# Kernel optimization log

Measured on AMD Instinct MI355X. Metric: run time of the kernel, lower is better.

## Reference

```python
import jax, jax.numpy as jnp
import numpy as np

D_IN = 768
D_OUT = 768
NUM_HEADS = 12
HEAD_DIM = D_OUT // NUM_HEADS
SEQ = 4096
BATCH = 1


def setup_inputs() -> dict:
    key = jax.random.key(0)
    ks = jax.random.split(key, 6)
    s = 1.0 / np.sqrt(D_IN)
    return {
        "x": jax.random.normal(ks[0], (BATCH, SEQ, D_IN), dtype=jnp.float32),
        "W_query": jax.random.normal(ks[1], (D_IN, D_OUT), dtype=jnp.float32) * s,
        "W_key": jax.random.normal(ks[2], (D_IN, D_OUT), dtype=jnp.float32) * s,
        "W_value": jax.random.normal(ks[3], (D_IN, D_OUT), dtype=jnp.float32) * s,
        "W_out": jax.random.normal(ks[4], (D_OUT, D_OUT), dtype=jnp.float32) * s,
        "b_out": jax.random.normal(ks[5], (D_OUT,), dtype=jnp.float32) * 0.01,
    }


def reference(x, W_query, W_key, W_value, W_out, b_out):
    B, S, _ = x.shape
    # QKV projections (qkv_bias=False)
    q = (x @ W_query).reshape(B, S, NUM_HEADS, HEAD_DIM)
    k = (x @ W_key).reshape(B, S, NUM_HEADS, HEAD_DIM)
    v = (x @ W_value).reshape(B, S, NUM_HEADS, HEAD_DIM)
    # attention scores [B, H, S, S] with causal mask
    scores = jnp.einsum("bqhd,bkhd->bhqk", q, k) / jnp.sqrt(
        jnp.asarray(HEAD_DIM, dtype=x.dtype)
    )
    causal = jnp.tril(jnp.ones((S, S), dtype=bool))
    scores = jnp.where(causal, scores, jnp.finfo(x.dtype).min)
    attn = jax.nn.softmax(scores, axis=-1)  # dropout p=0.0 -> identity
    ctx = jnp.einsum("bhqk,bkhd->bqhd", attn, v).reshape(B, S, D_OUT)
    return ctx @ W_out + b_out
```

## Files before the change

kernel.cpp:

```cpp
#include <hip/hip_runtime.h>
#include <stdint.h>

#define SEQ 4096
#define DM 768
#define NH 12
#define HD 64

typedef __attribute__((ext_vector_type(8))) short bf8;
typedef __attribute__((ext_vector_type(4))) float f4;
typedef __attribute__((ext_vector_type(16))) float f32x16;

static __device__ __forceinline__ f4 mfma_bf16(bf8 a, bf8 b, f4 c) {
  return __builtin_amdgcn_mfma_f32_16x16x32_bf16(a, b, c, 0, 0, 0);
}
static __device__ __forceinline__ f32x16 mfma32(bf8 a, bf8 b, f32x16 c) {
  return __builtin_amdgcn_mfma_f32_32x32x16_bf16(a, b, c, 0, 0, 0);
}

static __device__ __forceinline__ unsigned short f2bf(float f) {
  unsigned int u = __float_as_uint(f);
  u += 0x7FFFu + ((u >> 16) & 1u);
  return (unsigned short)(u >> 16);
}

static __device__ __forceinline__ unsigned int cvtpk(float lo, float hi) {
  unsigned int r;
  asm("v_cvt_pk_bf16_f32 %0, %1, %2" : "=v"(r) : "v"(lo), "v"(hi));
  return r;
}

static __device__ __forceinline__ void gload_lds16(const void* g, void* l) {
  __builtin_amdgcn_global_load_lds(
      (const __attribute__((address_space(1))) void*)g,
      (__attribute__((address_space(3))) void*)l, 16, 0, 0);
}

__global__ __launch_bounds__(256) void k_cvt(const float* __restrict__ x,
                                             unsigned short* __restrict__ xb) {
  int i = (blockIdx.x * 256 + threadIdx.x) * 4;
  float4 v = *reinterpret_cast<const float4*>(x + i);
  ushort4 o;
  o.x = f2bf(v.x); o.y = f2bf(v.y); o.z = f2bf(v.z); o.w = f2bf(v.w);
  *reinterpret_cast<ushort4*>(xb + i) = o;
}

__global__ __launch_bounds__(256) void k_tw(const float* __restrict__ w0,
                                            const float* __restrict__ w1,
                                            const float* __restrict__ w2,
                                            const float* __restrict__ w3,
                                            unsigned short* __restrict__ wt) {
  const float* W = blockIdx.z == 0 ? w0 : blockIdx.z == 1 ? w1
                 : blockIdx.z == 2 ? w2 : w3;
  unsigned short* WT = wt + (size_t)blockIdx.z * DM * DM;
  __shared__ float t[32][33];
  int c0 = blockIdx.x * 32, r0 = blockIdx.y * 32;
  int lx = threadIdx.x & 31, ly = threadIdx.x >> 5;
#pragma unroll
  for (int rr = 0; rr < 32; rr += 8)
    t[ly + rr][lx] = W[(size_t)(r0 + ly + rr) * DM + c0 + lx];
  __syncthreads();
#pragma unroll
  for (int rr = 0; rr < 32; rr += 8)
    WT[(size_t)(c0 + ly + rr) * DM + r0 + lx] = f2bf(t[lx][ly + rr]);
}

template <int MODE>
__global__ __launch_bounds__(256) void k_gemm(const unsigned short* __restrict__ A,
                                              const unsigned short* __restrict__ Bt,
                                              void* __restrict__ Cout,
                                              const float* __restrict__ bias,
                                              float scale) {
  constexpr int K = DM;
  __shared__ unsigned short sA[128 * 32];
  __shared__ unsigned short sB[64 * 32];
  const int t = threadIdx.x, lane = t & 63, w = t >> 6;
  const int wr = w >> 1, wc = w & 1;
  const int c = lane & 15, g = lane >> 4;
  const int brow = blockIdx.x * 128, bcol = blockIdx.y * 64;
  f4 acc[4][2] = {};
  for (int k0 = 0; k0 < K; k0 += 32) {
#pragma unroll
    for (int i = 0; i < 2; ++i) {
      int slot = w * 2 + i;
      int chunk = slot * 64 + lane;
      int row = chunk >> 2;
      int sl = (chunk & 3) ^ ((row >> 1) & 3);
      gload_lds16(A + (size_t)(brow + row) * K + k0 + sl * 8, &sA[slot * 512]);
    }
    {
      int chunk = w * 64 + lane;
      int row = chunk >> 2;
      int sl = (chunk & 3) ^ ((row >> 1) & 3);
      gload_lds16(Bt + (size_t)(bcol + row) * K + k0 + sl * 8, &sB[w * 512]);
    }
    __syncthreads();
    bf8 af[4], bfr[2];
#pragma unroll
    for (int m = 0; m < 4; ++m) {
      int row = wr * 64 + m * 16 + c;
      int off = row * 64 + ((g * 16) ^ (((row >> 1) & 3) << 4));
      af[m] = *reinterpret_cast<const bf8*>(reinterpret_cast<const char*>(sA) + off);
    }
#pragma unroll
    for (int n = 0; n < 2; ++n) {
      int row = wc * 32 + n * 16 + c;
      int off = row * 64 + ((g * 16) ^ (((row >> 1) & 3) << 4));
      bfr[n] = *reinterpret_cast<const bf8*>(reinterpret_cast<const char*>(sB) + off);
    }
#pragma unroll
    for (int m = 0; m < 4; ++m)
#pragma unroll
      for (int n = 0; n < 2; ++n)
        acc[m][n] = mfma_bf16(af[m], bfr[n], acc[m][n]);
    __syncthreads();
  }
#pragma unroll
  for (int m = 0; m < 4; ++m) {
#pragma unroll
    for (int n = 0; n < 2; ++n) {
      int col = bcol + wc * 32 + n * 16 + c;
      int row0 = brow + wr * 64 + m * 16 + g * 4;
      if (MODE == 0) {
        unsigned short* C = (unsigned short*)Cout;
        int h = col >> 6, d = col & 63;
#pragma unroll
        for (int r = 0; r < 4; ++r)
          C[((size_t)h * SEQ + row0 + r) * 64 + d] = f2bf(acc[m][n][r] * scale);
      } else if (MODE == 1) {
        unsigned short* C = (unsigned short*)Cout;
        ushort4 p;
        p.x = f2bf(acc[m][n][0]); p.y = f2bf(acc[m][n][1]);
        p.z = f2bf(acc[m][n][2]); p.w = f2bf(acc[m][n][3]);
        *reinterpret_cast<ushort4*>(C + (size_t)col * SEQ + row0) = p;
      } else {
        float* C = (float*)Cout;
#pragma unroll
        for (int r = 0; r < 4; ++r)
          C[(size_t)(row0 + r) * DM + col] = acc[m][n][r] + bias[col];
      }
    }
  }
}

#define PSWAP(a, b) asm volatile("v_permlane32_swap_b32 %0, %1" : "+v"(a), "+v"(b))

#define STAGEK(tile) do {                                                     \
    const unsigned short* ks_ = Khp + (size_t)(tile) * 4096 + kLaneOff;       \
    _Pragma("unroll")                                                         \
    for (int j_ = 0; j_ < 8; ++j_)                                            \
      gload_lds16(ks_ + j_ * 512, kbuf + j_ * 1024);                          \
  } while (0)

#define ALOADV8(a0, a1) do {                                                  \
    asm volatile("global_load_dwordx4 %0, %1, off"           : "=v"(vf[0]) : "v"(a0)); \
    asm volatile("global_load_dwordx4 %0, %1, off offset:32" : "=v"(vf[1]) : "v"(a0)); \
    asm volatile("global_load_dwordx4 %0, %1, off offset:64" : "=v"(vf[2]) : "v"(a0)); \
    asm volatile("global_load_dwordx4 %0, %1, off offset:96" : "=v"(vf[3]) : "v"(a0)); \
    asm volatile("global_load_dwordx4 %0, %1, off"           : "=v"(vf[4]) : "v"(a1)); \
    asm volatile("global_load_dwordx4 %0, %1, off offset:32" : "=v"(vf[5]) : "v"(a1)); \
    asm volatile("global_load_dwordx4 %0, %1, off offset:64" : "=v"(vf[6]) : "v"(a1)); \
    asm volatile("global_load_dwordx4 %0, %1, off offset:96" : "=v"(vf[7]) : "v"(a1)); \
  } while (0)

#define PBUILD(sv, pfx, pfy) do {                                             \
    float p0_ = __builtin_amdgcn_exp2f(sv[0] - mn_);                          \
    float p1_ = __builtin_amdgcn_exp2f(sv[1] - mn_);                          \
    float p2_ = __builtin_amdgcn_exp2f(sv[2] - mn_);                          \
    float p3_ = __builtin_amdgcn_exp2f(sv[3] - mn_);                          \
    float p4_ = __builtin_amdgcn_exp2f(sv[4] - mn_);                          \
    float p5_ = __builtin_amdgcn_exp2f(sv[5] - mn_);                          \
    float p6_ = __builtin_amdgcn_exp2f(sv[6] - mn_);                          \
    float p7_ = __builtin_amdgcn_exp2f(sv[7] - mn_);                          \
    unsigned int wa0_ = cvtpk(p0_, p1_), wa1_ = cvtpk(p2_, p3_);              \
    unsigned int wb0_ = cvtpk(p4_, p5_), wb1_ = cvtpk(p6_, p7_);              \
    ls_ += ((p0_ + p1_) + (p2_ + p3_)) + ((p4_ + p5_) + (p6_ + p7_));         \
    float q0_ = __builtin_amdgcn_exp2f(sv[8] - mn_);                          \
    float q1_ = __builtin_amdgcn_exp2f(sv[9] - mn_);                          \
    float q2_ = __builtin_amdgcn_exp2f(sv[10] - mn_);                         \
    float q3_ = __builtin_amdgcn_exp2f(sv[11] - mn_);                         \
    float q4_ = __builtin_amdgcn_exp2f(sv[12] - mn_);                         \
    float q5_ = __builtin_amdgcn_exp2f(sv[13] - mn_);                         \
    float q6_ = __builtin_amdgcn_exp2f(sv[14] - mn_);                         \
    float q7_ = __builtin_amdgcn_exp2f(sv[15] - mn_);                         \
    unsigned int wc0_ = cvtpk(q0_, q1_), wc1_ = cvtpk(q2_, q3_);              \
    unsigned int wd0_ = cvtpk(q4_, q5_), wd1_ = cvtpk(q6_, q7_);              \
    ls_ += ((q0_ + q1_) + (q2_ + q3_)) + ((q4_ + q5_) + (q6_ + q7_));         \
    PSWAP(wa0_, wb0_);                                                        \
    PSWAP(wa1_, wb1_);                                                        \
    PSWAP(wc0_, wd0_);                                                        \
    PSWAP(wc1_, wd1_);                                                        \
    uint4 u0_ = {wa0_, wa1_, wb0_, wb1_};                                     \
    uint4 u1_ = {wc0_, wc1_, wd0_, wd1_};                                     \
    pfx = *reinterpret_cast<bf8*>(&u0_);                                      \
    pfy = *reinterpret_cast<bf8*>(&u1_);                                      \
  } while (0)

#define STEP64(t) do {                                                        \
    bf8 vf[8];                                                                \
    const uint64_t va0_ = Vb0a + (uint64_t)(t) * 128;                         \
    const uint64_t va1_ = Vb1a + (uint64_t)(t) * 128;                         \
    ALOADV8(va0_, va1_);                                                      \
    asm volatile("s_waitcnt vmcnt(8)" ::: "memory");                          \
    f32x16 s0_ = {}, s1_ = {};                                                \
    {                                                                         \
      const char* kr0_ = kbuf + ql * 128;                                     \
      const char* kr1_ = kbuf + (32 + ql) * 128;                              \
      const int x0_ = ((hi) ^ xq) << 4;                                       \
      const int x1_ = ((2 + hi) ^ xq) << 4;                                   \
      const int x2_ = ((4 + hi) ^ xq) << 4;                                   \
      const int x3_ = ((6 + hi) ^ xq) << 4;                                   \
      bf8 ka0_ = *(const bf8*)(kr0_ + x0_);                                   \
      bf8 kb0_ = *(const bf8*)(kr1_ + x0_);                                   \
      bf8 ka1_ = *(const bf8*)(kr0_ + x1_);                                   \
      bf8 kb1_ = *(const bf8*)(kr1_ + x1_);                                   \
      bf8 ka2_ = *(const bf8*)(kr0_ + x2_);                                   \
      bf8 kb2_ = *(const bf8*)(kr1_ + x2_);                                   \
      bf8 ka3_ = *(const bf8*)(kr0_ + x3_);                                   \
      bf8 kb3_ = *(const bf8*)(kr1_ + x3_);                                   \
      __builtin_amdgcn_s_setprio(1);                                          \
      s0_ = mfma32(ka0_, qf[0], s0_);  s1_ = mfma32(kb0_, qf[0], s1_);        \
      s0_ = mfma32(ka1_, qf[1], s0_);  s1_ = mfma32(kb1_, qf[1], s1_);        \
      s0_ = mfma32(ka2_, qf[2], s0_);  s1_ = mfma32(kb2_, qf[2], s1_);        \
      s0_ = mfma32(ka3_, qf[3], s0_);  s1_ = mfma32(kb3_, qf[3], s1_);        \
      __builtin_amdgcn_s_setprio(0);                                          \
    }                                                                         \
    asm volatile("s_waitcnt lgkmcnt(0)" ::: "memory");                        \
    STAGEK((t) + 4);                                                          \
    if ((t) == dt) {                                                          \
      _Pragma("unroll")                                                       \
      for (int r_ = 0; r_ < 16; ++r_) {                                       \
        int kr_ = (t) * 64 + (r_ & 3) + 8 * (r_ >> 2) + 4 * hi;               \
        s0_[r_] = (kr_ > qg) ? -1e30f : s0_[r_];                              \
        s1_[r_] = (kr_ + 32 > qg) ? -1e30f : s1_[r_];                         \
      }                                                                       \
    }                                                                         \
    float tm_ = s0_[0];                                                       \
    _Pragma("unroll")                                                         \
    for (int r_ = 1; r_ < 16; ++r_) tm_ = fmaxf(tm_, s0_[r_]);                \
    _Pragma("unroll")                                                         \
    for (int r_ = 0; r_ < 16; ++r_) tm_ = fmaxf(tm_, s1_[r_]);                \
    tm_ = fmaxf(tm_, __shfl_xor(tm_, 32));                                    \
    float mn_ = fmaxf(m, tm_);                                                \
    float al_ = __builtin_amdgcn_exp2f(m - mn_);                              \
    m = mn_;                                                                  \
    float ls_ = 0.f;                                                          \
    bf8 pfA0_, pfA1_, pfB0_, pfB1_;                                           \
    PBUILD(s0_, pfA0_, pfA1_);                                                \
    PBUILD(s1_, pfB0_, pfB1_);                                                \
    ls_ += __shfl_xor(ls_, 32);                                               \
    l = l * al_ + ls_;                                                        \
    _Pragma("unroll")                                                         \
    for (int r_ = 0; r_ < 16; ++r_) { o0[r_] *= al_; o1[r_] *= al_; }         \
    asm volatile("s_waitcnt vmcnt(8)" ::: "memory");                          \
    __builtin_amdgcn_sched_barrier(0);                                        \
    __builtin_amdgcn_s_setprio(1);                                            \
    o0 = mfma32(vf[0], pfA0_, o0);                                            \
    o0 = mfma32(vf[1], pfA1_, o0);                                            \
    o0 = mfma32(vf[2], pfB0_, o0);                                            \
    o0 = mfma32(vf[3], pfB1_, o0);                                            \
    o1 = mfma32(vf[4], pfA0_, o1);                                            \
    o1 = mfma32(vf[5], pfA1_, o1);                                            \
    o1 = mfma32(vf[6], pfB0_, o1);                                            \
    o1 = mfma32(vf[7], pfB1_, o1);                                            \
    __builtin_amdgcn_s_setprio(0);                                            \
  } while (0)

__global__ __launch_bounds__(256, 3) void k_attn(const unsigned short* __restrict__ Qh,
                                                 const unsigned short* __restrict__ Kh,
                                                 const unsigned short* __restrict__ Vt,
                                                 unsigned short* __restrict__ ctx) {
  const int tid = threadIdx.x;
  const int lane = tid & 63;
  const int w = tid >> 6;
  const int ql = lane & 31, hi = lane >> 5;
  const int xq = ql & 7;

  const int L = (int)blockIdx.x;
  const int W = (L & 7) * 96 + (L >> 3);
  const int h = W >> 6;
  const int b = W & 63;
  const size_t hd = (size_t)h * HD;

  __shared__ char smem[33792];
  char* kbuf = smem + w * 8192;
  float* sO = (float*)smem;
  float* sM = (float*)(smem + 32768);
  float* sL = (float*)(smem + 33280);

  const unsigned short* Khp = Kh + (size_t)h * SEQ * 64;
  const unsigned short* Qhp = Qh + (size_t)h * SEQ * 64;
  const int kLaneOff = (lane >> 3) * 64 + ((lane & 7) ^ (lane >> 3)) * 8;
  const uint64_t Vb0base = (uint64_t)(Vt + (hd + ql) * SEQ + hi * 8);
  const uint64_t Vb1base = Vb0base + (uint64_t)32 * SEQ * 2;

  for (int ph = 0; ph < 2; ++ph) {
    const int qt = ph ? (127 - b) : b;
    const int qg = qt * 32 + ql;
    const int dt = qt >> 1;
    bf8 qf[4];
    {
      const unsigned short* qp = Qhp + (size_t)qg * 64 + hi * 8;
      qf[0] = *reinterpret_cast<const bf8*>(qp);
      qf[1] = *reinterpret_cast<const bf8*>(qp + 16);
      qf[2] = *reinterpret_cast<const bf8*>(qp + 32);
      qf[3] = *reinterpret_cast<const bf8*>(qp + 48);
    }
    f32x16 o0 = {}, o1 = {};
    float m = -1e30f, l = 0.f;
    const uint64_t Vb0a = Vb0base, Vb1a = Vb1base;

    const int nt = (dt >= w) ? ((dt - w) >> 2) + 1 : 0;
    if (nt > 0) {
      STAGEK(w);
      for (int i = 0; i < nt; ++i) {
        const int t = w + 4 * i;
        STEP64(t);
      }
    }
    asm volatile("s_waitcnt vmcnt(0)" ::: "memory");

#pragma unroll
    for (int r = 0; r < 16; ++r) {
      int dr = (r & 3) + 8 * (r >> 2) + 4 * hi;
      sO[w * 2048 + dr * 32 + ql] = o0[r];
      sO[w * 2048 + (32 + dr) * 32 + ql] = o1[r];
    }
    if (hi == 0) { sM[w * 32 + ql] = m; sL[w * 32 + ql] = l; }
    __syncthreads();
    {
      const int q = tid & 31;
      const int dblk = tid >> 5;
      float m0 = sM[q], m1 = sM[32 + q], m2 = sM[64 + q], m3 = sM[96 + q];
      float mn = fmaxf(fmaxf(m0, m1), fmaxf(m2, m3));
      float a0 = __builtin_amdgcn_exp2f(m0 - mn);
      float a1 = __builtin_amdgcn_exp2f(m1 - mn);
      float a2 = __builtin_amdgcn_exp2f(m2 - mn);
      float a3 = __builtin_amdgcn_exp2f(m3 - mn);
      float inv = 1.f / (a0 * sL[q] + a1 * sL[32 + q] + a2 * sL[64 + q] + a3 * sL[96 + q]);
      a0 *= inv; a1 *= inv; a2 *= inv; a3 *= inv;
      unsigned short* cp = ctx + (size_t)(qt * 32 + q) * DM + hd + dblk * 8;
#pragma unroll
      for (int j = 0; j < 8; j += 2) {
        int d = dblk * 8 + j;
        float v0 = sO[d * 32 + q] * a0 + sO[2048 + d * 32 + q] * a1 +
                   sO[4096 + d * 32 + q] * a2 + sO[6144 + d * 32 + q] * a3;
        float v1 = sO[(d + 1) * 32 + q] * a0 + sO[2048 + (d + 1) * 32 + q] * a1 +
                   sO[4096 + (d + 1) * 32 + q] * a2 + sO[6144 + (d + 1) * 32 + q] * a3;
        *reinterpret_cast<unsigned int*>(cp + j) = cvtpk(v0, v1);
      }
    }
    __syncthreads();
  }
}

extern "C" void kernel_launch(void* const* d_in, const int* in_sizes, int n_in,
                              void* d_out, int out_size, void* d_ws, size_t ws_size,
                              hipStream_t stream) {
  const float* x  = (const float*)d_in[0];
  const float* Wq = (const float*)d_in[1];
  const float* Wk = (const float*)d_in[2];
  const float* Wv = (const float*)d_in[3];
  const float* Wo = (const float*)d_in[4];
  const float* bo = (const float*)d_in[5];

  unsigned short* xb = (unsigned short*)d_ws;
  unsigned short* wt = xb + (size_t)SEQ * DM;
  unsigned short* Qh = wt + (size_t)4 * DM * DM;
  unsigned short* Kh = Qh + (size_t)SEQ * DM;
  unsigned short* Vt = Kh + (size_t)SEQ * DM;
  unsigned short* cx = Vt + (size_t)SEQ * DM;

  const float qscale = 1.4426950408889634f / 8.0f;

  k_cvt<<<(SEQ * DM) / 1024, 256, 0, stream>>>(x, xb);
  k_tw<<<dim3(24, 24, 4), 256, 0, stream>>>(Wq, Wk, Wv, Wo, wt);
  dim3 gg(SEQ / 128, DM / 64);
  k_gemm<0><<<gg, 256, 0, stream>>>(xb, wt, Qh, nullptr, qscale);
  k_gemm<0><<<gg, 256, 0, stream>>>(xb, wt + (size_t)DM * DM, Kh, nullptr, 1.0f);
  k_gemm<1><<<gg, 256, 0, stream>>>(xb, wt + (size_t)2 * DM * DM, Vt, nullptr, 1.0f);
  k_attn<<<dim3(768), 256, 0, stream>>>(Qh, Kh, Vt, cx);
  k_gemm<2><<<gg, 256, 0, stream>>>(cx, wt + (size_t)3 * DM * DM, d_out, bo, 1.0f);
}
```

Baseline: 135.7 us.

## Stage V tiles through LDS with async loads alongside K in attention

The V-projection GEMM now writes V in a tiled per-head layout of 64x64 blocks, so each key tile of V is contiguous. The attention kernel now stages both K and V tiles into per-wave LDS buffers with direct global-to-LDS loads, prefetching the next tile after the current fragments are read. Previously V fragments were loaded with strided direct global loads. The change also skips the redundant prefetch on the last iteration, uses a tree max reduction, and lowers the occupancy hint from 3 to 2 because shared memory doubles to about 65KB.

```diff
diff --git a/kernel.cpp b/kernel.cpp
--- a/kernel.cpp
+++ b/kernel.cpp
@@ -128,10 +128,12 @@
           C[((size_t)h * SEQ + row0 + r) * 64 + d] = f2bf(acc[m][n][r] * scale);
       } else if (MODE == 1) {
         unsigned short* C = (unsigned short*)Cout;
+        int h = col >> 6, d = col & 63;
         ushort4 p;
         p.x = f2bf(acc[m][n][0]); p.y = f2bf(acc[m][n][1]);
         p.z = f2bf(acc[m][n][2]); p.w = f2bf(acc[m][n][3]);
-        *reinterpret_cast<ushort4*>(C + (size_t)col * SEQ + row0) = p;
+        *reinterpret_cast<ushort4*>(
+            C + ((((size_t)h * 64 + (row0 >> 6)) * 64 + d) * 64 + (row0 & 63))) = p;
       } else {
         float* C = (float*)Cout;
 #pragma unroll
@@ -143,23 +145,13 @@
 }
 
 #define PSWAP(a, b) asm volatile("v_permlane32_swap_b32 %0, %1" : "+v"(a), "+v"(b))
-
-#define STAGEK(tile) do {                                                     \
-    const unsigned short* ks_ = Khp + (size_t)(tile) * 4096 + kLaneOff;       \
+#define SGB() __builtin_amdgcn_sched_barrier(0)
+
+#define STAGE8K(srcbase, tile, dst) do {                                      \
+    const unsigned short* s_ = (srcbase) + (size_t)(tile) * 4096 + kLaneOff;  \
     _Pragma("unroll")                                                         \
     for (int j_ = 0; j_ < 8; ++j_)                                            \
-      gload_lds16(ks_ + j_ * 512, kbuf + j_ * 1024);                          \
-  } while (0)
-
-#define ALOADV8(a0, a1) do {                                                  \
-    asm volatile("global_load_dwordx4 %0, %1, off"           : "=v"(vf[0]) : "v"(a0)); \
-    asm volatile("global_load_dwordx4 %0, %1, off offset:32" : "=v"(vf[1]) : "v"(a0)); \
-    asm volatile("global_load_dwordx4 %0, %1, off offset:64" : "=v"(vf[2]) : "v"(a0)); \
-    asm volatile("global_load_dwordx4 %0, %1, off offset:96" : "=v"(vf[3]) : "v"(a0)); \
-    asm volatile("global_load_dwordx4 %0, %1, off"           : "=v"(vf[4]) : "v"(a1)); \
-    asm volatile("global_load_dwordx4 %0, %1, off offset:32" : "=v"(vf[5]) : "v"(a1)); \
-    asm volatile("global_load_dwordx4 %0, %1, off offset:64" : "=v"(vf[6]) : "v"(a1)); \
-    asm volatile("global_load_dwordx4 %0, %1, off offset:96" : "=v"(vf[7]) : "v"(a1)); \
+      gload_lds16(s_ + j_ * 512, (dst) + j_ * 1024);                          \
   } while (0)
 
 #define PBUILD(sv, pfx, pfy) do {                                             \
@@ -195,37 +187,37 @@
     pfy = *reinterpret_cast<bf8*>(&u1_);                                      \
   } while (0)
 
-#define STEP64(t) do {                                                        \
-    bf8 vf[8];                                                                \
-    const uint64_t va0_ = Vb0a + (uint64_t)(t) * 128;                         \
-    const uint64_t va1_ = Vb1a + (uint64_t)(t) * 128;                         \
-    ALOADV8(va0_, va1_);                                                      \
-    asm volatile("s_waitcnt vmcnt(8)" ::: "memory");                          \
+#define FMAX8(v, i0) fmaxf(fmaxf(fmaxf(v[i0], v[i0+1]), fmaxf(v[i0+2], v[i0+3])), \
+                           fmaxf(fmaxf(v[i0+4], v[i0+5]), fmaxf(v[i0+6], v[i0+7])))
+
+#define STEP64(t, stage_) do {                                                \
+    asm volatile("s_waitcnt vmcnt(0)" ::: "memory");                          \
+    SGB();                                                                    \
+    const int x0_ = ((hi) ^ xq) << 4;                                         \
+    const int x1_ = ((2 + hi) ^ xq) << 4;                                     \
+    const int x2_ = ((4 + hi) ^ xq) << 4;                                     \
+    const int x3_ = ((6 + hi) ^ xq) << 4;                                     \
+    const char* kr0_ = kbuf + ql * 128;                                       \
+    const char* kr1_ = kbuf + (32 + ql) * 128;                                \
+    bf8 ka0_ = *(const bf8*)(kr0_ + x0_);                                     \
+    bf8 kb0_ = *(const bf8*)(kr1_ + x0_);                                     \
+    bf8 ka1_ = *(const bf8*)(kr0_ + x1_);                                     \
+    bf8 kb1_ = *(const bf8*)(kr1_ + x1_);                                     \
+    bf8 ka2_ = *(const bf8*)(kr0_ + x2_);                                     \
+    bf8 kb2_ = *(const bf8*)(kr1_ + x2_);                                     \
+    bf8 ka3_ = *(const bf8*)(kr0_ + x3_);                                     \
+    bf8 kb3_ = *(const bf8*)(kr1_ + x3_);                                     \
+    SGB();                                                                    \
+    asm volatile("s_waitcnt lgkmcnt(0)" ::: "memory");                        \
+    SGB();                                                                    \
+    if (stage_) STAGE8K(Khp, (t) + 4, kbuf);                                  \
     f32x16 s0_ = {}, s1_ = {};                                                \
-    {                                                                         \
-      const char* kr0_ = kbuf + ql * 128;                                     \
-      const char* kr1_ = kbuf + (32 + ql) * 128;                              \
-      const int x0_ = ((hi) ^ xq) << 4;                                       \
-      const int x1_ = ((2 + hi) ^ xq) << 4;                                   \
-      const int x2_ = ((4 + hi) ^ xq) << 4;                                   \
-      const int x3_ = ((6 + hi) ^ xq) << 4;                                   \
-      bf8 ka0_ = *(const bf8*)(kr0_ + x0_);                                   \
-      bf8 kb0_ = *(const bf8*)(kr1_ + x0_);                                   \
-      bf8 ka1_ = *(const bf8*)(kr0_ + x1_);                                   \
-      bf8 kb1_ = *(const bf8*)(kr1_ + x1_);                                   \
-      bf8 ka2_ = *(const bf8*)(kr0_ + x2_);                                   \
-      bf8 kb2_ = *(const bf8*)(kr1_ + x2_);                                   \
-      bf8 ka3_ = *(const bf8*)(kr0_ + x3_);                                   \
-      bf8 kb3_ = *(const bf8*)(kr1_ + x3_);                                   \
-      __builtin_amdgcn_s_setprio(1);                                          \
-      s0_ = mfma32(ka0_, qf[0], s0_);  s1_ = mfma32(kb0_, qf[0], s1_);        \
-      s0_ = mfma32(ka1_, qf[1], s0_);  s1_ = mfma32(kb1_, qf[1], s1_);        \
-      s0_ = mfma32(ka2_, qf[2], s0_);  s1_ = mfma32(kb2_, qf[2], s1_);        \
-      s0_ = mfma32(ka3_, qf[3], s0_);  s1_ = mfma32(kb3_, qf[3], s1_);        \
-      __builtin_amdgcn_s_setprio(0);                                          \
-    }                                                                         \
-    asm volatile("s_waitcnt lgkmcnt(0)" ::: "memory");                        \
-    STAGEK((t) + 4);                                                          \
+    __builtin_amdgcn_s_setprio(1);                                            \
+    s0_ = mfma32(ka0_, qf[0], s0_);  s1_ = mfma32(kb0_, qf[0], s1_);          \
+    s0_ = mfma32(ka1_, qf[1], s0_);  s1_ = mfma32(kb1_, qf[1], s1_);          \
+    s0_ = mfma32(ka2_, qf[2], s0_);  s1_ = mfma32(kb2_, qf[2], s1_);          \
+    s0_ = mfma32(ka3_, qf[3], s0_);  s1_ = mfma32(kb3_, qf[3], s1_);          \
+    __builtin_amdgcn_s_setprio(0);                                            \
     if ((t) == dt) {                                                          \
       _Pragma("unroll")                                                       \
       for (int r_ = 0; r_ < 16; ++r_) {                                       \
@@ -234,11 +226,8 @@
         s1_[r_] = (kr_ + 32 > qg) ? -1e30f : s1_[r_];                         \
       }                                                                       \
     }                                                                         \
-    float tm_ = s0_[0];                                                       \
-    _Pragma("unroll")                                                         \
-    for (int r_ = 1; r_ < 16; ++r_) tm_ = fmaxf(tm_, s0_[r_]);                \
-    _Pragma("unroll")                                                         \
-    for (int r_ = 0; r_ < 16; ++r_) tm_ = fmaxf(tm_, s1_[r_]);                \
+    float tm_ = fmaxf(fmaxf(FMAX8(s0_, 0), FMAX8(s0_, 8)),                    \
+                      fmaxf(FMAX8(s1_, 0), FMAX8(s1_, 8)));                   \
     tm_ = fmaxf(tm_, __shfl_xor(tm_, 32));                                    \
     float mn_ = fmaxf(m, tm_);                                                \
     float al_ = __builtin_amdgcn_exp2f(m - mn_);                              \
@@ -249,23 +238,35 @@
     PBUILD(s1_, pfB0_, pfB1_);                                                \
     ls_ += __shfl_xor(ls_, 32);                                               \
     l = l * al_ + ls_;                                                        \
+    const char* vr0_ = vbuf + ql * 128;                                       \
+    const char* vr1_ = vbuf + (32 + ql) * 128;                                \
+    bf8 va0_ = *(const bf8*)(vr0_ + x0_);                                     \
+    bf8 va1_ = *(const bf8*)(vr0_ + x1_);                                     \
+    bf8 va2_ = *(const bf8*)(vr0_ + x2_);                                     \
+    bf8 va3_ = *(const bf8*)(vr0_ + x3_);                                     \
+    bf8 vb0_ = *(const bf8*)(vr1_ + x0_);                                     \
+    bf8 vb1_ = *(const bf8*)(vr1_ + x1_);                                     \
+    bf8 vb2_ = *(const bf8*)(vr1_ + x2_);                                     \
+    bf8 vb3_ = *(const bf8*)(vr1_ + x3_);                                     \
+    SGB();                                                                    \
+    asm volatile("s_waitcnt lgkmcnt(0)" ::: "memory");                        \
+    SGB();                                                                    \
+    if (stage_) STAGE8K(Vtp, (t) + 4, vbuf);                                  \
     _Pragma("unroll")                                                         \
     for (int r_ = 0; r_ < 16; ++r_) { o0[r_] *= al_; o1[r_] *= al_; }         \
-    asm volatile("s_waitcnt vmcnt(8)" ::: "memory");                          \
-    __builtin_amdgcn_sched_barrier(0);                                        \
     __builtin_amdgcn_s_setprio(1);                                            \
-    o0 = mfma32(vf[0], pfA0_, o0);                                            \
-    o0 = mfma32(vf[1], pfA1_, o0);                                            \
-    o0 = mfma32(vf[2], pfB0_, o0);                                            \
-    o0 = mfma32(vf[3], pfB1_, o0);                                            \
-    o1 = mfma32(vf[4], pfA0_, o1);                                            \
-    o1 = mfma32(vf[5], pfA1_, o1);                                            \
-    o1 = mfma32(vf[6], pfB0_, o1);                                            \
-    o1 = mfma32(vf[7], pfB1_, o1);                                            \
+    o0 = mfma32(va0_, pfA0_, o0);                                             \
+    o0 = mfma32(va1_, pfA1_, o0);                                             \
+    o0 = mfma32(va2_, pfB0_, o0);                                             \
+    o0 = mfma32(va3_, pfB1_, o0);                                             \
+    o1 = mfma32(vb0_, pfA0_, o1);                                             \
+    o1 = mfma32(vb1_, pfA1_, o1);                                             \
+    o1 = mfma32(vb2_, pfB0_, o1);                                             \
+    o1 = mfma32(vb3_, pfB1_, o1);                                             \
     __builtin_amdgcn_s_setprio(0);                                            \
   } while (0)
 
-__global__ __launch_bounds__(256, 3) void k_attn(const unsigned short* __restrict__ Qh,
+__global__ __launch_bounds__(256, 2) void k_attn(const unsigned short* __restrict__ Qh,
                                                  const unsigned short* __restrict__ Kh,
                                                  const unsigned short* __restrict__ Vt,
                                                  unsigned short* __restrict__ ctx) {
@@ -279,19 +280,18 @@
   const int W = (L & 7) * 96 + (L >> 3);
   const int h = W >> 6;
   const int b = W & 63;
-  const size_t hd = (size_t)h * HD;
-
-  __shared__ char smem[33792];
+
+  __shared__ __align__(16) char smem[66560];
   char* kbuf = smem + w * 8192;
+  char* vbuf = smem + 32768 + w * 8192;
   float* sO = (float*)smem;
-  float* sM = (float*)(smem + 32768);
-  float* sL = (float*)(smem + 33280);
+  float* sM = (float*)(smem + 65536);
+  float* sL = (float*)(smem + 66048);
 
   const unsigned short* Khp = Kh + (size_t)h * SEQ * 64;
   const unsigned short* Qhp = Qh + (size_t)h * SEQ * 64;
+  const unsigned short* Vtp = Vt + (size_t)h * SEQ * 64;
   const int kLaneOff = (lane >> 3) * 64 + ((lane & 7) ^ (lane >> 3)) * 8;
-  const uint64_t Vb0base = (uint64_t)(Vt + (hd + ql) * SEQ + hi * 8);
-  const uint64_t Vb1base = Vb0base + (uint64_t)32 * SEQ * 2;
 
   for (int ph = 0; ph < 2; ++ph) {
     const int qt = ph ? (127 - b) : b;
@@ -307,17 +307,17 @@
     }
     f32x16 o0 = {}, o1 = {};
     float m = -1e30f, l = 0.f;
-    const uint64_t Vb0a = Vb0base, Vb1a = Vb1base;
 
     const int nt = (dt >= w) ? ((dt - w) >> 2) + 1 : 0;
     if (nt > 0) {
-      STAGEK(w);
+      STAGE8K(Khp, w, kbuf);
+      STAGE8K(Vtp, w, vbuf);
       for (int i = 0; i < nt; ++i) {
         const int t = w + 4 * i;
-        STEP64(t);
+        STEP64(t, (i + 1 < nt));
       }
     }
-    asm volatile("s_waitcnt vmcnt(0)" ::: "memory");
+    __syncthreads();
 
 #pragma unroll
     for (int r = 0; r < 16; ++r) {
@@ -338,7 +338,7 @@
       float a3 = __builtin_amdgcn_exp2f(m3 - mn);
       float inv = 1.f / (a0 * sL[q] + a1 * sL[32 + q] + a2 * sL[64 + q] + a3 * sL[96 + q]);
       a0 *= inv; a1 *= inv; a2 *= inv; a3 *= inv;
-      unsigned short* cp = ctx + (size_t)(qt * 32 + q) * DM + hd + dblk * 8;
+      unsigned short* cp = ctx + (size_t)(qt * 32 + q) * DM + h * HD + dblk * 8;
 #pragma unroll
       for (int j = 0; j < 8; j += 2) {
         int d = dblk * 8 + j;
```

New measurement: 124.3 us. -8.4%, faster.
